# Kernel tuning notes

Measured on AMD Instinct MI355X. Metric: run time of the kernel, lower is better.

## Reference

```python
import jax, jax.numpy as jnp
import numpy as np

EMBED_DIM = 1024
SEQ_LEN = 2048
BATCH = 4


def setup_inputs() -> dict:
    key = jax.random.key(0)
    kx, kq, kk, kv = jax.random.split(key, 4)
    scale = 1.0 / np.sqrt(EMBED_DIM)
    x = jax.random.normal(kx, (BATCH, SEQ_LEN, EMBED_DIM), dtype=jnp.float32)
    # nn.Linear weights are [out, in]; stored transposed-application here
    W_query = jax.random.normal(kq, (EMBED_DIM, EMBED_DIM), dtype=jnp.float32) * scale
    W_key = jax.random.normal(kk, (EMBED_DIM, EMBED_DIM), dtype=jnp.float32) * scale
    W_value = jax.random.normal(kv, (EMBED_DIM, EMBED_DIM), dtype=jnp.float32) * scale
    return {"x": x, "W_query": W_query, "W_key": W_key, "W_value": W_value}


def reference(x, W_query, W_key, W_value):
    # x: [B, S, D]; W_*: [D_out, D_in] (torch nn.Linear layout -> y = x @ W.T)
    B, S, D = x.shape
    q = jnp.einsum("bsd,ed->bse", x, W_query)
    k = jnp.einsum("bsd,ed->bse", x, W_key)
    v = jnp.einsum("bsd,ed->bse", x, W_value)
    scores = jnp.einsum("bqd,bkd->bqk", q, k)  # [B, S, S]
    causal = jnp.triu(jnp.ones((S, S), dtype=bool), k=1)  # True above diagonal
    scores = jnp.where(causal, -jnp.inf, scores)
    weights = jax.nn.softmax(scores / jnp.sqrt(jnp.asarray(D, x.dtype)), axis=-1)
    return jnp.einsum("bqk,bkd->bqd", weights, v)
```

## Files before the change

### kernel.cpp

```cpp
#include <hip/hip_runtime.h>
#include <stdint.h>

typedef __bf16 bf16_t;
typedef __bf16 bf16x4 __attribute__((ext_vector_type(4)));
typedef __bf16 bf16x8 __attribute__((ext_vector_type(8)));
typedef float  f32x4  __attribute__((ext_vector_type(4)));

#define AS1 __attribute__((address_space(1)))
#define AS3 __attribute__((address_space(3)))

__device__ __forceinline__ void gld_lds16(const bf16_t* g, void* s) {
  __builtin_amdgcn_global_load_lds((const AS1 uint32_t*)g, (AS3 uint32_t*)s, 16, 0, 0);
}

__global__ __launch_bounds__(256) void convert_all_kernel(
    const float* __restrict__ X,  const float* __restrict__ Wq,
    const float* __restrict__ Wk, const float* __restrict__ Wv,
    bf16_t* __restrict__ Xc, bf16_t* __restrict__ Wqc,
    bf16_t* __restrict__ Wkc, bf16_t* __restrict__ Wvc) {
  const int blk = blockIdx.x;
  const float* src; bf16_t* dst; int base;
  if (blk < 4096)      { src = X;  dst = Xc;  base = 0;    }
  else if (blk < 4608) { src = Wq; dst = Wqc; base = 4096; }
  else if (blk < 5120) { src = Wk; dst = Wkc; base = 4608; }
  else                 { src = Wv; dst = Wvc; base = 5120; }
  const int i = ((blk - base) * 256 + threadIdx.x) * 8;
  const float4 a = ((const float4*)(src + i))[0];
  const float4 b = ((const float4*)(src + i))[1];
  bf16x8 v;
  v[0] = (bf16_t)a.x; v[1] = (bf16_t)a.y; v[2] = (bf16_t)a.z; v[3] = (bf16_t)a.w;
  v[4] = (bf16_t)b.x; v[5] = (bf16_t)b.y; v[6] = (bf16_t)b.z; v[7] = (bf16_t)b.w;
  *(bf16x8*)(dst + i) = v;
}

__device__ __forceinline__ void gemm_bt_core(
    const bf16_t* __restrict__ A, int lda,
    const bf16_t* __restrict__ B, int ldb,
    int m0, int n0, int kBeg, int kEnd,
    bf16_t* As, bf16_t* Bs, f32x4 acc[4][4])
{
  const int lane = threadIdx.x & 63;
  const int wave = threadIdx.x >> 6;
  const int wm = (wave >> 1) * 64;
  const int wn = (wave & 1) * 64;
  const int fr = lane & 15;
  const int ck = lane >> 4;

  const int srow = lane >> 3;
  const int sch  = lane & 7;

  int grow[4], kg[4], dst[4];
#pragma unroll
  for (int j = 0; j < 4; ++j) {
    const int r = wave * 32 + j * 8 + srow;
    grow[j] = r;
    kg[j]   = (sch ^ (r & 7)) * 8;
    dst[j]  = r * 128 + sch * 16;
  }

  int aoff[4][2], boff[4][2];
#pragma unroll
  for (int i = 0; i < 4; ++i) {
    const int ra = wm + i * 16 + fr;
    const int rb = wn + i * 16 + fr;
#pragma unroll
    for (int kh = 0; kh < 2; ++kh) {
      aoff[i][kh] = ra * 128 + (((kh * 4 + ck) ^ (ra & 7)) * 16);
      boff[i][kh] = rb * 128 + (((kh * 4 + ck) ^ (rb & 7)) * 16);
    }
  }

  for (int kt = kBeg; kt < kEnd; kt += 64) {
    __syncthreads();
#pragma unroll
    for (int j = 0; j < 4; ++j) {
      gld_lds16(A + (size_t)(m0 + grow[j]) * lda + kt + kg[j], (char*)As + dst[j]);
      gld_lds16(B + (size_t)(n0 + grow[j]) * ldb + kt + kg[j], (char*)Bs + dst[j]);
    }
    __syncthreads();

    bf16x8 af[4][2], bfv[4][2];
#pragma unroll
    for (int i = 0; i < 4; ++i)
#pragma unroll
      for (int kh = 0; kh < 2; ++kh) {
        af[i][kh]  = *(const bf16x8*)((char*)As + aoff[i][kh]);
        bfv[i][kh] = *(const bf16x8*)((char*)Bs + boff[i][kh]);
      }
#pragma unroll
    for (int kh = 0; kh < 2; ++kh)
#pragma unroll
      for (int mi = 0; mi < 4; ++mi)
#pragma unroll
        for (int ni = 0; ni < 4; ++ni)
          acc[mi][ni] = __builtin_amdgcn_mfma_f32_16x16x32_bf16(
              af[mi][kh], bfv[ni][kh], acc[mi][ni], 0, 0, 0);
  }
}

__global__ __launch_bounds__(256) void qkv_kernel(
    const bf16_t* __restrict__ X,
    const bf16_t* __restrict__ Wq, const bf16_t* __restrict__ Wk,
    const bf16_t* __restrict__ Wv,
    bf16_t* __restrict__ Q, bf16_t* __restrict__ K, bf16_t* __restrict__ Vt)
{
  __shared__ bf16_t smem[2 * 128 * 64];
  bf16_t* As = smem;
  bf16_t* Bs = smem + 128 * 64;
  const int m0 = blockIdx.x * 128;
  const int n0 = blockIdx.y * 128;
  const int z  = blockIdx.z;
  const bf16_t* W = (z == 0) ? Wq : (z == 1) ? Wk : Wv;

  f32x4 acc[4][4] = {};
  gemm_bt_core(X, 1024, W, 1024, m0, n0, 0, 1024, As, Bs, acc);

  const int lane = threadIdx.x & 63;
  const int wave = threadIdx.x >> 6;
  const int wm = (wave >> 1) * 64, wn = (wave & 1) * 64;

  if (z < 2) {
    bf16_t* Out = z ? K : Q;
#pragma unroll
    for (int mi = 0; mi < 4; ++mi)
#pragma unroll
      for (int r = 0; r < 4; ++r) {
        const int row = m0 + wm + mi * 16 + (lane >> 4) * 4 + r;
#pragma unroll
        for (int ni = 0; ni < 4; ++ni) {
          const int col = n0 + wn + ni * 16 + (lane & 15);
          Out[(size_t)row * 1024 + col] = (bf16_t)acc[mi][ni][r];
        }
      }
  } else {
    const int b  = m0 >> 11;
    const int s0 = m0 & 2047;
    bf16_t* Vtb = Vt + (size_t)b * 1024 * 2048;
    bf16_t (*t)[136] = (bf16_t(*)[136])smem;
#pragma unroll
    for (int h = 0; h < 2; ++h) {
      __syncthreads();
      if ((wave & 1) == h) {
#pragma unroll
        for (int mi = 0; mi < 4; ++mi)
#pragma unroll
          for (int ni = 0; ni < 4; ++ni) {
            const int c   = ni * 16 + (lane & 15);
            const int row = wm + mi * 16 + (lane >> 4) * 4;
            bf16x4 v;
            v[0] = (bf16_t)acc[mi][ni][0]; v[1] = (bf16_t)acc[mi][ni][1];
            v[2] = (bf16_t)acc[mi][ni][2]; v[3] = (bf16_t)acc[mi][ni][3];
            *(bf16x4*)&t[c][row] = v;
          }
      }
      __syncthreads();
#pragma unroll
      for (int i = 0; i < 4; ++i) {
        const int u  = threadIdx.x + 256 * i;
        const int d  = u >> 4;
        const int ch = u & 15;
        bf16x8 vv = *(const bf16x8*)&t[d][ch * 8];
        *(bf16x8*)(Vtb + (size_t)(n0 + h * 64 + d) * 2048 + s0 + ch * 8) = vv;
      }
    }
  }
}

__global__ __launch_bounds__(256) void scores_exp_kernel(
    const bf16_t* __restrict__ Q, const bf16_t* __restrict__ K,
    bf16_t* __restrict__ P, float* __restrict__ partials)
{
  const int kt = blockIdx.x;
  const int mt = blockIdx.y;
  if (kt > mt) return;
  const int m0 = mt * 128;
  const int n0 = kt * 128;
  __shared__ bf16_t smem[2 * 128 * 64];
  __shared__ float rowsum[2][128];
  bf16_t* As = smem;
  bf16_t* Bs = smem + 128 * 64;
  const int batch = blockIdx.z;
  const bf16_t* Qb = Q + (size_t)batch * 2048 * 1024;
  const bf16_t* Kb = K + (size_t)batch * 2048 * 1024;
  bf16_t* Pb = P + (size_t)batch * 2048 * 2048;
  float* lp  = partials + ((size_t)batch * 16 + kt) * 2048;

  f32x4 acc[4][4] = {};
  gemm_bt_core(Qb, 1024, Kb, 1024, m0, n0, 0, 1024, As, Bs, acc);

  const int lane = threadIdx.x & 63;
  const int wave = threadIdx.x >> 6;
  const int wm = (wave >> 1) * 64, wn = (wave & 1) * 64;
  const float c = 0.04508422f;
#pragma unroll
  for (int mi = 0; mi < 4; ++mi)
#pragma unroll
    for (int r = 0; r < 4; ++r) {
      const int lrow = wm + mi * 16 + (lane >> 4) * 4 + r;
      const int row  = m0 + lrow;
      float rs = 0.f;
#pragma unroll
      for (int ni = 0; ni < 4; ++ni) {
        const int col = n0 + wn + ni * 16 + (lane & 15);
        float p = exp2f(acc[mi][ni][r] * c);
        if (col > row) p = 0.f;
        const bf16_t pb = (bf16_t)p;
        Pb[(size_t)row * 2048 + col] = pb;
        rs += (float)pb;
      }
      rs += __shfl_xor(rs, 1);
      rs += __shfl_xor(rs, 2);
      rs += __shfl_xor(rs, 4);
      rs += __shfl_xor(rs, 8);
      if ((lane & 15) == 0) rowsum[wave & 1][lrow] = rs;
    }
  __syncthreads();
  if (threadIdx.x < 128)
    lp[m0 + threadIdx.x] = rowsum[0][threadIdx.x] + rowsum[1][threadIdx.x];
}

__global__ __launch_bounds__(256) void lsum_kernel(
    const float* __restrict__ partials, float* __restrict__ Linv)
{
  const int id  = blockIdx.x * 256 + threadIdx.x;
  const int z   = id >> 11;
  const int row = id & 2047;
  const float* lp = partials + (size_t)z * 16 * 2048;
  const int tmax = row >> 7;
  float l = 0.f;
  for (int kt = 0; kt <= tmax; ++kt) l += lp[kt * 2048 + row];
  Linv[id] = 1.f / l;
}

__global__ __launch_bounds__(256) void pv_kernel(
    const bf16_t* __restrict__ P, const bf16_t* __restrict__ Vt,
    const float* __restrict__ Linv, float* __restrict__ out)
{
  __shared__ bf16_t smem[2 * 128 * 64];
  bf16_t* As = smem;
  bf16_t* Bs = smem + 128 * 64;
  const int zb = blockIdx.z;
  const int mt = ((zb >> 1) & 1) ? (15 - blockIdx.y) : blockIdx.y;
  const int m0 = mt * 128;
  const int n0 = blockIdx.x * 128;
  const bf16_t* Pb  = P  + (size_t)zb * 2048 * 2048;
  const bf16_t* Vtb = Vt + (size_t)zb * 1024 * 2048;
  const float* li = Linv + (size_t)zb * 2048;
  float* ob = out + (size_t)zb * 2048 * 1024;

  f32x4 acc[4][4] = {};
  gemm_bt_core(Pb, 2048, Vtb, 2048, m0, n0, 0, m0 + 128, As, Bs, acc);

  const int lane = threadIdx.x & 63;
  const int wave = threadIdx.x >> 6;
  const int wm = (wave >> 1) * 64, wn = (wave & 1) * 64;
#pragma unroll
  for (int mi = 0; mi < 4; ++mi)
#pragma unroll
    for (int r = 0; r < 4; ++r) {
      const int row = m0 + wm + mi * 16 + (lane >> 4) * 4 + r;
      const float inv = li[row];
#pragma unroll
      for (int ni = 0; ni < 4; ++ni) {
        const int col = n0 + wn + ni * 16 + (lane & 15);
        ob[(size_t)row * 1024 + col] = acc[mi][ni][r] * inv;
      }
    }
}

extern "C" void kernel_launch(void* const* d_in, const int* in_sizes, int n_in,
                              void* d_out, int out_size, void* d_ws, size_t ws_size,
                              hipStream_t stream) {
  const float* X  = (const float*)d_in[0];
  const float* Wq = (const float*)d_in[1];
  const float* Wk = (const float*)d_in[2];
  const float* Wv = (const float*)d_in[3];
  float* out = (float*)d_out;
  char* ws = (char*)d_ws;

  const size_t MB = 1024 * 1024;
  bf16_t* Q    = (bf16_t*)(ws + 0 * MB);
  bf16_t* K    = (bf16_t*)(ws + 16 * MB);
  bf16_t* Vt   = (bf16_t*)(ws + 32 * MB);
  bf16_t* Xc   = (bf16_t*)(ws + 48 * MB);
  bf16_t* Wqc  = (bf16_t*)(ws + 64 * MB);
  bf16_t* Wkc  = (bf16_t*)(ws + 66 * MB);
  bf16_t* Wvc  = (bf16_t*)(ws + 68 * MB);
  bf16_t* P    = (bf16_t*)(ws + 48 * MB);
  float*  Lp   = (float*)(ws + 80 * MB);
  float*  Linv = (float*)(ws + 80 * MB + 512 * 1024);

  convert_all_kernel<<<dim3(5632), 256, 0, stream>>>(X, Wq, Wk, Wv, Xc, Wqc, Wkc, Wvc);
  qkv_kernel<<<dim3(64, 8, 3), 256, 0, stream>>>(Xc, Wqc, Wkc, Wvc, Q, K, Vt);
  scores_exp_kernel<<<dim3(16, 16, 4), 256, 0, stream>>>(Q, K, P, Lp);
  lsum_kernel<<<dim3(32), 256, 0, stream>>>(Lp, Linv);
  pv_kernel<<<dim3(8, 16, 4), 256, 0, stream>>>(P, Vt, Linv, out);
}
```

Baseline: 251.5 us.

## Double-buffer LDS in GEMM core with K-tile 32 and MFMA priority

Rewrites the shared GEMM core to use two LDS buffers with a K-step of 32, prefetching the next tile via global_load_lds while the current tile's MFMAs run, so each iteration needs one barrier instead of two. The swizzle pattern is adapted to 64-byte rows, and s_setprio raises wave priority around the MFMA block. This aims to hide global-load latency, at the cost of twice as many loop iterations and reliance on the async LDS loads completing by the next barrier.

```diff
diff --git a/kernel.cpp b/kernel.cpp
--- a/kernel.cpp
+++ b/kernel.cpp
@@ -46,55 +46,57 @@
   const int fr = lane & 15;
   const int ck = lane >> 4;
 
-  const int srow = lane >> 3;
-  const int sch  = lane & 7;
-
-  int grow[4], kg[4], dst[4];
-#pragma unroll
-  for (int j = 0; j < 4; ++j) {
-    const int r = wave * 32 + j * 8 + srow;
-    grow[j] = r;
-    kg[j]   = (sch ^ (r & 7)) * 8;
-    dst[j]  = r * 128 + sch * 16;
-  }
-
-  int aoff[4][2], boff[4][2];
+  const int off0 = wave * 2048 + lane * 16;
+  const int row0 = wave * 32 + (lane >> 2);
+  const int row1 = row0 + 16;
+  const int kg   = ((lane & 3) ^ ((row0 >> 1) & 3)) * 8;
+
+  const bf16_t* Ar0 = A + (size_t)(m0 + row0) * lda + kg;
+  const bf16_t* Ar1 = A + (size_t)(m0 + row1) * lda + kg;
+  const bf16_t* Br0 = B + (size_t)(n0 + row0) * ldb + kg;
+  const bf16_t* Br1 = B + (size_t)(n0 + row1) * ldb + kg;
+
+  int aoff[4], boff[4];
 #pragma unroll
   for (int i = 0; i < 4; ++i) {
     const int ra = wm + i * 16 + fr;
     const int rb = wn + i * 16 + fr;
-#pragma unroll
-    for (int kh = 0; kh < 2; ++kh) {
-      aoff[i][kh] = ra * 128 + (((kh * 4 + ck) ^ (ra & 7)) * 16);
-      boff[i][kh] = rb * 128 + (((kh * 4 + ck) ^ (rb & 7)) * 16);
+    aoff[i] = ra * 64 + ((ck ^ ((ra >> 1) & 3)) * 16);
+    boff[i] = rb * 64 + ((ck ^ ((rb >> 1) & 3)) * 16);
+  }
+
+  gld_lds16(Ar0 + kBeg, (char*)As + off0);
+  gld_lds16(Ar1 + kBeg, (char*)As + off0 + 1024);
+  gld_lds16(Br0 + kBeg, (char*)Bs + off0);
+  gld_lds16(Br1 + kBeg, (char*)Bs + off0 + 1024);
+  __syncthreads();
+
+  int cur = 0;
+  for (int kt = kBeg; kt < kEnd; kt += 32) {
+    const int nxt = cur ^ 1;
+    if (kt + 32 < kEnd) {
+      gld_lds16(Ar0 + kt + 32, (char*)As + nxt * 8192 + off0);
+      gld_lds16(Ar1 + kt + 32, (char*)As + nxt * 8192 + off0 + 1024);
+      gld_lds16(Br0 + kt + 32, (char*)Bs + nxt * 8192 + off0);
+      gld_lds16(Br1 + kt + 32, (char*)Bs + nxt * 8192 + off0 + 1024);
     }
-  }
-
-  for (int kt = kBeg; kt < kEnd; kt += 64) {
+    bf16x8 af[4], bfv[4];
+#pragma unroll
+    for (int mi = 0; mi < 4; ++mi)
+      af[mi] = *(const bf16x8*)((char*)As + cur * 8192 + aoff[mi]);
+#pragma unroll
+    for (int ni = 0; ni < 4; ++ni)
+      bfv[ni] = *(const bf16x8*)((char*)Bs + cur * 8192 + boff[ni]);
+    __builtin_amdgcn_s_setprio(1);
+#pragma unroll
+    for (int mi = 0; mi < 4; ++mi)
+#pragma unroll
+      for (int ni = 0; ni < 4; ++ni)
+        acc[mi][ni] = __builtin_amdgcn_mfma_f32_16x16x32_bf16(
+            af[mi], bfv[ni], acc[mi][ni], 0, 0, 0);
+    __builtin_amdgcn_s_setprio(0);
     __syncthreads();
-#pragma unroll
-    for (int j = 0; j < 4; ++j) {
-      gld_lds16(A + (size_t)(m0 + grow[j]) * lda + kt + kg[j], (char*)As + dst[j]);
-      gld_lds16(B + (size_t)(n0 + grow[j]) * ldb + kt + kg[j], (char*)Bs + dst[j]);
-    }
-    __syncthreads();
-
-    bf16x8 af[4][2], bfv[4][2];
-#pragma unroll
-    for (int i = 0; i < 4; ++i)
-#pragma unroll
-      for (int kh = 0; kh < 2; ++kh) {
-        af[i][kh]  = *(const bf16x8*)((char*)As + aoff[i][kh]);
-        bfv[i][kh] = *(const bf16x8*)((char*)Bs + boff[i][kh]);
-      }
-#pragma unroll
-    for (int kh = 0; kh < 2; ++kh)
-#pragma unroll
-      for (int mi = 0; mi < 4; ++mi)
-#pragma unroll
-        for (int ni = 0; ni < 4; ++ni)
-          acc[mi][ni] = __builtin_amdgcn_mfma_f32_16x16x32_bf16(
-              af[mi][kh], bfv[ni][kh], acc[mi][ni], 0, 0, 0);
+    cur = nxt;
   }
 }
 
@@ -104,9 +106,9 @@
     const bf16_t* __restrict__ Wv,
     bf16_t* __restrict__ Q, bf16_t* __restrict__ K, bf16_t* __restrict__ Vt)
 {
-  __shared__ bf16_t smem[2 * 128 * 64];
+  __shared__ bf16_t smem[4 * 128 * 32];
   bf16_t* As = smem;
-  bf16_t* Bs = smem + 128 * 64;
+  bf16_t* Bs = smem + 2 * 128 * 32;
   const int m0 = blockIdx.x * 128;
   const int n0 = blockIdx.y * 128;
   const int z  = blockIdx.z;
@@ -175,10 +177,10 @@
   if (kt > mt) return;
   const int m0 = mt * 128;
   const int n0 = kt * 128;
-  __shared__ bf16_t smem[2 * 128 * 64];
+  __shared__ bf16_t smem[4 * 128 * 32];
   __shared__ float rowsum[2][128];
   bf16_t* As = smem;
-  bf16_t* Bs = smem + 128 * 64;
+  bf16_t* Bs = smem + 2 * 128 * 32;
   const int batch = blockIdx.z;
   const bf16_t* Qb = Q + (size_t)batch * 2048 * 1024;
   const bf16_t* Kb = K + (size_t)batch * 2048 * 1024;
@@ -236,9 +238,9 @@
     const bf16_t* __restrict__ P, const bf16_t* __restrict__ Vt,
     const float* __restrict__ Linv, float* __restrict__ out)
 {
-  __shared__ bf16_t smem[2 * 128 * 64];
+  __shared__ bf16_t smem[4 * 128 * 32];
   bf16_t* As = smem;
-  bf16_t* Bs = smem + 128 * 64;
+  bf16_t* Bs = smem + 2 * 128 * 32;
   const int zb = blockIdx.z;
   const int mt = ((zb >> 1) & 1) ? (15 - blockIdx.y) : blockIdx.y;
   const int m0 = mt * 128;
```

Result: no change. 250.2 us (-0.5%).
